# Kernel optimization log

Hardware: AMD Instinct MI355X
Metric: run time of the kernel (lower is better)

## Reference

```python
import jax, jax.numpy as jnp
import numpy as np

N_HEAD = 16
THETA = 10000.0


def _freqs_cos_sin(head_dim, seq_len):
    # matches precompute_freqs_cis: freqs = 1/theta^(arange(0,dim,2)/dim), outer with t
    inv = 1.0 / (THETA ** (jnp.arange(0, head_dim, 2, dtype=jnp.float32) / head_dim))
    t = jnp.arange(seq_len, dtype=jnp.float32)
    ang = jnp.outer(t, inv)  # [L, head_dim//2]
    return jnp.cos(ang), jnp.sin(ang)


def _rope(x, cos, sin):
    # x: [B, H, L, D]; pairs are interleaved (view_as_complex on (..., D//2, 2))
    x1 = x[..., 0::2]
    x2 = x[..., 1::2]
    out_re = x1 * cos - x2 * sin
    out_im = x1 * sin + x2 * cos
    return jnp.stack([out_re, out_im], axis=-1).reshape(x.shape)


def setup_inputs() -> dict:
    key = jax.random.key(0)
    ks = jax.random.split(key, 11)
    B, L, D = 2, 2048, 1024
    s = 0.02
    return {
        "q": jax.random.normal(ks[0], (B, L, D), jnp.float32),
        "k": jax.random.normal(ks[1], (B, L, D), jnp.float32),
        "v": jax.random.normal(ks[2], (B, L, D), jnp.float32),
        "wq": jax.random.normal(ks[3], (D, D), jnp.float32) * s,
        "bq": jax.random.normal(ks[4], (D,), jnp.float32) * s,
        "wk": jax.random.normal(ks[5], (D, D), jnp.float32) * s,
        "bk": jax.random.normal(ks[6], (D,), jnp.float32) * s,
        "wv": jax.random.normal(ks[7], (D, D), jnp.float32) * s,
        "bv": jax.random.normal(ks[8], (D,), jnp.float32) * s,
        "wo": jax.random.normal(ks[9], (D, D), jnp.float32) * s,
        "bo": jax.random.normal(ks[10], (D,), jnp.float32) * s,
    }


def reference(q, k, v, wq, bq, wk, bk, wv, bv, wo, bo):
    B, L, D = q.shape
    Hd = D // N_HEAD
    # projections (nn.Linear: x @ W^T + b)
    qp = q @ wq.T + bq
    kp = k @ wk.T + bk
    vp = v @ wv.T + bv
    # split: [B, L, D] -> [B, H, L, Hd]
    def split(t):
        return t.reshape(B, L, N_HEAD, Hd).transpose(0, 2, 1, 3)
    qh, kh, vh = split(qp), split(kp), split(vp)
    cos, sin = _freqs_cos_sin(Hd, L)  # [L, Hd//2], broadcasts over B, H
    qh = _rope(qh, cos, sin)
    kh = _rope(kh, cos, sin)
    # scaled dot-product attention (no mask)
    scores = jnp.einsum("bhqd,bhkd->bhqk", qh, kh) / jnp.sqrt(jnp.float32(Hd))
    attn = jax.nn.softmax(scores, axis=-1)
    out = jnp.einsum("bhqk,bhkd->bhqd", attn, vh)
    # concat heads and output projection
    out = out.transpose(0, 2, 1, 3).reshape(B, L, D)
    return out @ wo.T + bo
```

## Files before the change

### kernel.cpp

```cpp
#include <hip/hip_runtime.h>
#include <hip/hip_bf16.h>
#include <math.h>

#define BB 2
#define LL 2048
#define DD 1024
#define NH 16
#define HD 64

typedef short v8s __attribute__((ext_vector_type(8)));
typedef float v4f __attribute__((ext_vector_type(4)));
typedef float v16f __attribute__((ext_vector_type(16)));

__device__ __forceinline__ float b2f(unsigned short b) {
  union { unsigned int u; float f; } c; c.u = ((unsigned int)b) << 16; return c.f;
}
__device__ __forceinline__ unsigned short f2b(float x) {
  union { float f; unsigned int u; } c; c.f = x;
  unsigned int u = c.u;
  u += 0x7fffu + ((u >> 16) & 1u);
  return (unsigned short)(u >> 16);
}
__device__ __forceinline__ unsigned int asu(float x) {
  union { float f; unsigned int u; } c; c.f = x; return c.u;
}
__device__ __forceinline__ unsigned int pk2(float lo, float hi) {
  return __builtin_amdgcn_perm(asu(hi), asu(lo), 0x07060302u);
}

#if defined(__has_builtin)
#if __has_builtin(__builtin_amdgcn_exp2f)
#define EXP2(x) __builtin_amdgcn_exp2f(x)
#else
#define EXP2(x) __expf((x) * 0.69314718056f)
#endif
#else
#define EXP2(x) __expf((x) * 0.69314718056f)
#endif

__device__ __forceinline__ void gload16(const void* g, void* l) {
  __builtin_amdgcn_global_load_lds(
      (const __attribute__((address_space(1))) void*)g,
      (__attribute__((address_space(3))) void*)l, 16, 0, 0);
}

#define VM_WAIT4 do { asm volatile("s_waitcnt vmcnt(4)" ::: "memory"); \
                      __builtin_amdgcn_sched_barrier(0); } while (0)
#define VM_WAIT0 do { asm volatile("s_waitcnt vmcnt(0)" ::: "memory"); \
                      __builtin_amdgcn_sched_barrier(0); } while (0)
#define SBAR     do { __builtin_amdgcn_s_barrier(); \
                      __builtin_amdgcn_sched_barrier(0); } while (0)

struct CastArgs { const float* s[7]; unsigned short* d[7]; float* ct; float* st; };
__global__ void cast_all(CastArgs a) {
  int z = blockIdx.z;
  if (z == 16) {
    if (blockIdx.x >= 256) return;
    int id = blockIdx.x * blockDim.x + threadIdx.x;
    int t = id >> 5, i = id & 31;
    float inv = powf(10000.0f, -(float)(2 * i) / 64.0f);
    float ang = (float)t * inv;
    a.ct[id] = cosf(ang);
    a.st[id] = sinf(ang);
    return;
  }
  int t = (z < 12) ? (z >> 2) : (z - 9);
  int off = (z < 12) ? ((z & 3) << 18) : 0;
  int i = off + blockIdx.x * blockDim.x + threadIdx.x;
  float4 v = ((const float4*)a.s[t])[i];
  ushort4 o;
  o.x = f2b(v.x); o.y = f2b(v.y); o.z = f2b(v.z); o.w = f2b(v.w);
  ((ushort4*)a.d[t])[i] = o;
}

__device__ __forceinline__ size_t ring_src_off(int id, int row0, int Kd) {
  int sr = id >> 3, slot = id & 7;
  int g = slot ^ (sr & 7);
  int r = (sr << 1) | (g >> 2), c = g & 3;
  return (size_t)(row0 + r) * Kd + c * 8;
}
__device__ __forceinline__ int ring_frag_off(int row, int quad) {
  int sr = row >> 1;
  int slot = (((row & 1) << 2) | quad) ^ (sr & 7);
  return sr * 64 + slot * 8;
}

__device__ __forceinline__ void ring_gemm_core(
    const unsigned short* __restrict__ X, const unsigned short* __restrict__ W,
    unsigned short* LDS_, int bm0, int bn0, v4f acc[4][4]) {
  const int K = DD;
  const int tid = threadIdx.x;
  const int lane = tid & 63, wave = tid >> 6;
  const int quad = lane >> 4, l16 = lane & 15;
  const int wm = (wave >> 1) * 64, wn = (wave & 1) * 64;

  const unsigned short* aS0 = X + ring_src_off(tid, bm0, K);
  const unsigned short* aS1 = X + ring_src_off(256 + tid, bm0, K);
  const unsigned short* bS0 = W + ring_src_off(tid, bn0, K);
  const unsigned short* bS1 = W + ring_src_off(256 + tid, bn0, K);

  int aoff[4], boff[4];
#pragma unroll
  for (int i = 0; i < 4; ++i) {
    aoff[i] = ring_frag_off(wm + i * 16 + l16, quad);
    boff[i] = ring_frag_off(wn + i * 16 + l16, quad);
  }

  auto stage = [&](int q, int kofs) {
    unsigned short* Ab = &LDS_[q * 4096];
    unsigned short* Bb = &LDS_[12288 + q * 4096];
    gload16(aS0 + kofs, &Ab[tid * 8]);
    gload16(aS1 + kofs, &Ab[(256 + tid) * 8]);
    gload16(bS0 + kofs, &Bb[tid * 8]);
    gload16(bS1 + kofs, &Bb[(256 + tid) * 8]);
  };
  auto compute = [&](int q) {
    const unsigned short* Ab = &LDS_[q * 4096];
    const unsigned short* Bb = &LDS_[12288 + q * 4096];
    v8s a[4], b[4];
#pragma unroll
    for (int i = 0; i < 4; ++i) {
      a[i] = *(const v8s*)&Ab[aoff[i]];
      b[i] = *(const v8s*)&Bb[boff[i]];
    }
#pragma unroll
    for (int mi = 0; mi < 4; ++mi)
#pragma unroll
      for (int ni = 0; ni < 4; ++ni)
        acc[mi][ni] = __builtin_amdgcn_mfma_f32_16x16x32_bf16(a[mi], b[ni], acc[mi][ni], 0, 0, 0);
  };

  const int nt = K / 32;
  stage(0, 0);
  stage(1, 32);
  VM_WAIT4;
  SBAR;
  int cur = 0, s2 = 2, kofs = 64;
#pragma unroll 1
  for (int t = 0; t < nt - 2; ++t) {
    stage(s2, kofs);
    compute(cur);
    VM_WAIT4;
    SBAR;
    cur = (cur == 2) ? 0 : cur + 1;
    s2 = (s2 == 2) ? 0 : s2 + 1;
    kofs += 32;
  }
  compute(cur);
  VM_WAIT0;
  SBAR;
  cur = (cur == 2) ? 0 : cur + 1;
  compute(cur);
}

__global__ __launch_bounds__(256, 3) void gemm_qkv(
    const unsigned short* __restrict__ qb, const unsigned short* __restrict__ kb,
    const unsigned short* __restrict__ vb,
    const unsigned short* __restrict__ wqb, const unsigned short* __restrict__ wkb,
    const unsigned short* __restrict__ wvb,
    const float* __restrict__ bq, const float* __restrict__ bk,
    const float* __restrict__ bv_,
    unsigned short* __restrict__ qp, unsigned short* __restrict__ khh,
    unsigned short* __restrict__ vt,
    const float* __restrict__ ctab, const float* __restrict__ stab) {
  __shared__ __align__(16) unsigned short LDS_[24576];
  const int z = blockIdx.z;
  const unsigned short* X = (z == 0) ? qb : (z == 1) ? kb : vb;
  const unsigned short* W = (z == 0) ? wqb : (z == 1) ? wkb : wvb;
  const float* bias = (z == 0) ? bq : (z == 1) ? bk : bv_;
  const int N = DD;
  const int tid = threadIdx.x;
  const int lane = tid & 63, wave = tid >> 6;
  const int quad = lane >> 4, l16 = lane & 15;
  const int bm0 = blockIdx.x * 128;
  const int bn0 = blockIdx.y * 128;
  const int wm = (wave >> 1) * 64, wn = (wave & 1) * 64;

  const v4f vzero = {0.f, 0.f, 0.f, 0.f};
  v4f acc[4][4];
#pragma unroll
  for (int i = 0; i < 4; ++i)
#pragma unroll
    for (int j = 0; j < 4; ++j) acc[i][j] = vzero;

  ring_gemm_core(X, W, LDS_, bm0, bn0, acc);

  float bv[4];
#pragma unroll
  for (int ni = 0; ni < 4; ++ni) bv[ni] = bias[bn0 + wn + ni * 16 + l16];

  if (z < 2) {
    const float scl = (z == 0) ? 0.18033688f : 1.0f;
    const int h = (bn0 + wn) >> 6;
    const float sgn = (l16 & 1) ? 1.0f : -1.0f;
#pragma unroll
    for (int mi = 0; mi < 4; ++mi) {
#pragma unroll
      for (int r = 0; r < 4; ++r) {
        int row = bm0 + wm + mi * 16 + quad * 4 + r;
        int l = row & (LL - 1);
        int bidx = row >> 11;
        size_t baseq = (size_t)row * N + bn0 + wn + l16;
        size_t basek = ((size_t)(bidx * NH + h) * LL + l) * HD + l16;
#pragma unroll
        for (int ni = 0; ni < 4; ++ni) {
          int ii = (ni * 16 + l16) >> 1;
          float c = ctab[l * 32 + ii], s = stab[l * 32 + ii];
          float v = acc[mi][ni][r] + bv[ni];
          float vp = __shfl_xor(v, 1);
          float o = (v * c + sgn * (vp * s)) * scl;
          if (z == 0) qp[baseq + ni * 16] = f2b(o);
          else        khh[basek + ni * 16] = f2b(o);
        }
      }
    }
  } else {
    __syncthreads();
    unsigned short* T = LDS_;
#pragma unroll
    for (int mi = 0; mi < 4; ++mi)
#pragma unroll
      for (int r = 0; r < 4; ++r) {
        int tl = wm + mi * 16 + quad * 4 + r;
        int tlp = (tl & ~12) | ((tl & 4) << 1) | ((tl & 8) >> 1);
        int chunk = tlp >> 3, offw = tlp & 7;
#pragma unroll
        for (int ni = 0; ni < 4; ++ni) {
          int fl = wn + ni * 16 + l16;
          T[fl * 128 + ((chunk ^ (fl & 15)) * 8) + offw] =
              f2b(acc[mi][ni][r] + bv[ni]);
        }
      }
    __syncthreads();
    int fl = tid >> 1, half = tid & 1;
    int fg = bn0 + fl;
    int h2 = fg >> 6, d = fg & 63;
    int bidx = bm0 >> 11, l0 = bm0 & (LL - 1);
    unsigned short* dst =
        vt + (((size_t)(bidx * NH + h2) * HD + d) * LL) + l0 + half * 64;
#pragma unroll
    for (int i = 0; i < 8; ++i) {
      int chunk = half * 8 + i;
      int slot = chunk ^ (fl & 15);
      *(v8s*)(dst + i * 8) = *(const v8s*)&T[fl * 128 + slot * 8];
    }
  }
}

__global__ __launch_bounds__(256, 3) void gemm_out(
    const unsigned short* __restrict__ x, const unsigned short* __restrict__ w,
    const float* __restrict__ b, float* __restrict__ y) {
  __shared__ __align__(16) unsigned short LDS_[24576];
  const int N = DD;
  const int tid = threadIdx.x;
  const int lane = tid & 63, wave = tid >> 6;
  const int quad = lane >> 4, l16 = lane & 15;
  const int bm0 = blockIdx.x * 128;
  const int bn0 = blockIdx.y * 128;
  const int wm = (wave >> 1) * 64, wn = (wave & 1) * 64;

  const v4f vzero = {0.f, 0.f, 0.f, 0.f};
  v4f acc[4][4];
#pragma unroll
  for (int i = 0; i < 4; ++i)
#pragma unroll
    for (int j = 0; j < 4; ++j) acc[i][j] = vzero;

  ring_gemm_core(x, w, LDS_, bm0, bn0, acc);

  float bv[4];
#pragma unroll
  for (int ni = 0; ni < 4; ++ni) bv[ni] = b[bn0 + wn + ni * 16 + l16];
#pragma unroll
  for (int mi = 0; mi < 4; ++mi) {
#pragma unroll
    for (int r = 0; r < 4; ++r) {
      int row = bm0 + wm + mi * 16 + quad * 4 + r;
      size_t base = (size_t)row * N + bn0 + wn + l16;
#pragma unroll
      for (int ni = 0; ni < 4; ++ni)
        y[base + ni * 16] = acc[mi][ni][r] + bv[ni];
    }
  }
}

__global__ __launch_bounds__(256, 3) void flash_kernel(
    const unsigned short* __restrict__ qp,
    const unsigned short* __restrict__ kh,
    const unsigned short* __restrict__ vt,
    unsigned short* __restrict__ attn) {
  __shared__ __align__(16) unsigned short S_[24576];
  const int tid = threadIdx.x, wave = tid >> 6, lane = tid & 63;
  const int l32 = lane & 31, hf = lane >> 5;
  const int bh = blockIdx.x, b = bh >> 4, hd = bh & 15;
  const int q0 = blockIdx.y * 128;
  const unsigned short* kbase = kh + (size_t)bh * LL * HD;
  const unsigned short* vbase = vt + (size_t)bh * HD * LL;

  const int qrow = q0 + wave * 32 + l32;
  v8s qf[4];
  {
    const unsigned short* qsrc = qp + ((size_t)(b * LL + qrow) * DD + hd * HD);
#pragma unroll
    for (int ks2 = 0; ks2 < 4; ++ks2)
      qf[ks2] = *(const v8s*)(qsrc + ks2 * 16 + hf * 8);
  }

  const int r0 = tid >> 3, s0 = tid & 7;
  const int r1 = (256 + tid) >> 3;
  const unsigned short* kS0 = kbase + (size_t)r0 * HD + (s0 ^ (r0 & 7)) * 8;
  const unsigned short* kS1 = kbase + (size_t)r1 * HD + (s0 ^ (r1 & 7)) * 8;
  const unsigned short* vS0 = vbase + (size_t)r0 * LL + (s0 ^ (r0 & 7)) * 8;
  const unsigned short* vS1 = vbase + (size_t)r1 * LL + (s0 ^ (r1 & 7)) * 8;

  v16f o0, o1;
#pragma unroll
  for (int i = 0; i < 16; ++i) { o0[i] = 0.0f; o1[i] = 0.0f; }
  float ls = 0.0f;

  auto stage = [&](int q, int t) {
    unsigned short* Kb = &S_[q * 8192];
    unsigned short* Vb = &S_[q * 8192 + 4096];
    gload16(kS0 + (size_t)t * 4096, &Kb[tid * 8]);
    gload16(kS1 + (size_t)t * 4096, &Kb[(256 + tid) * 8]);
    gload16(vS0 + t * 64, &Vb[tid * 8]);
    gload16(vS1 + t * 64, &Vb[(256 + tid) * 8]);
  };

  auto compute = [&](int q) {
    const unsigned short* Ks = &S_[q * 8192];
    const unsigned short* Vs = &S_[q * 8192 + 4096];
#pragma unroll
    for (int g = 0; g < 2; ++g) {
      v16f sc;
#pragma unroll
      for (int i = 0; i < 16; ++i) sc[i] = 0.0f;
#pragma unroll
      for (int ks2 = 0; ks2 < 4; ++ks2) {
        int row = g * 32 + l32;
        int slot = (ks2 * 2 + hf) ^ (row & 7);
        v8s kf = *(const v8s*)&Ks[row * 64 + slot * 8];
        sc = __builtin_amdgcn_mfma_f32_32x32x16_bf16(kf, qf[ks2], sc, 0, 0, 0);
      }
      v16f e;
#pragma unroll
      for (int i = 0; i < 16; ++i) e[i] = EXP2(sc[i]);
      float t0 = (e[0] + e[1]) + (e[2] + e[3]);
      float t1 = (e[4] + e[5]) + (e[6] + e[7]);
      float t2 = (e[8] + e[9]) + (e[10] + e[11]);
      float t3 = (e[12] + e[13]) + (e[14] + e[15]);
      ls += (t0 + t1) + (t2 + t3);
#pragma unroll
      for (int k2 = 0; k2 < 2; ++k2) {
        union { v8s v; unsigned int u[4]; } pb;
#pragma unroll
        for (int a = 0; a < 4; ++a)
          pb.u[a] = pk2(e[8 * k2 + 2 * a], e[8 * k2 + 2 * a + 1]);
        int k16 = g * 2 + k2;
        int slotv = (k16 * 2 + hf) ^ (l32 & 7);
        v8s vf0 = *(const v8s*)&Vs[l32 * 64 + slotv * 8];
        v8s vf1 = *(const v8s*)&Vs[(32 + l32) * 64 + slotv * 8];
        o0 = __builtin_amdgcn_mfma_f32_32x32x16_bf16(vf0, pb.v, o0, 0, 0, 0);
        o1 = __builtin_amdgcn_mfma_f32_32x32x16_bf16(vf1, pb.v, o1, 0, 0, 0);
      }
    }
  };

  const int nt = LL / 64;
  stage(0, 0);
  stage(1, 1);
  VM_WAIT4;
  SBAR;
  int cur = 0, s2 = 2;
#pragma unroll 1
  for (int t = 0; t < nt - 2; ++t) {
    stage(s2, t + 2);
    compute(cur);
    VM_WAIT4;
    SBAR;
    cur = (cur == 2) ? 0 : cur + 1;
    s2 = (s2 == 2) ? 0 : s2 + 1;
  }
  compute(cur);
  VM_WAIT0;
  SBAR;
  cur = (cur == 2) ? 0 : cur + 1;
  compute(cur);

  ls += __shfl_xor(ls, 32);
  float inv = 1.0f / ls;

  unsigned short* Wt = S_ + wave * 2048;
#pragma unroll
  for (int dt = 0; dt < 2; ++dt)
#pragma unroll
    for (int r = 0; r < 16; ++r) {
      int dl = (r & 3) + 8 * (r >> 2) + 4 * hf;
      int d = dt * 32 + dl;
      int chunk = d >> 3, offw = d & 7;
      int slot = chunk ^ (l32 & 7);
      float val = (dt == 0) ? o0[r] : o1[r];
      Wt[l32 * 64 + slot * 8 + offw] = f2b(val * inv);
    }
#pragma unroll
  for (int i = 0; i < 4; ++i) {
    int qr = lane >> 1;
    int chunk = (lane & 1) * 4 + i;
    int slot = chunk ^ (qr & 7);
    v8s dv = *(const v8s*)&Wt[qr * 64 + slot * 8];
    int token = q0 + wave * 32 + qr;
    *(v8s*)(attn + ((size_t)(b * LL + token) * DD) + hd * HD + chunk * 8) = dv;
  }
}

extern "C" void kernel_launch(void* const* d_in, const int* in_sizes, int n_in,
                              void* d_out, int out_size, void* d_ws, size_t ws_size,
                              hipStream_t stream) {
  const float* q  = (const float*)d_in[0];
  const float* k  = (const float*)d_in[1];
  const float* v  = (const float*)d_in[2];
  const float* wq = (const float*)d_in[3];
  const float* bq = (const float*)d_in[4];
  const float* wk = (const float*)d_in[5];
  const float* bk = (const float*)d_in[6];
  const float* wv = (const float*)d_in[7];
  const float* bv = (const float*)d_in[8];
  const float* wo = (const float*)d_in[9];
  const float* bo = (const float*)d_in[10];
  float* out = (float*)d_out;

  size_t off = 0;
  char* wsb = (char*)d_ws;
  auto take = [&](size_t n) { void* p = wsb + off; off += n; return p; };
  const size_t SZT = (size_t)BB * LL * DD * 2;
  const size_t SZW = (size_t)DD * DD * 2;
  unsigned short* qb   = (unsigned short*)take(SZT);
  unsigned short* kb   = (unsigned short*)take(SZT);
  unsigned short* vb   = (unsigned short*)take(SZT);
  unsigned short* wqb  = (unsigned short*)take(SZW);
  unsigned short* wkb  = (unsigned short*)take(SZW);
  unsigned short* wvb  = (unsigned short*)take(SZW);
  unsigned short* wob  = (unsigned short*)take(SZW);
  unsigned short* qp   = (unsigned short*)take(SZT);
  unsigned short* khh  = (unsigned short*)take(SZT);
  unsigned short* vtt  = (unsigned short*)take(SZT);
  unsigned short* attn = (unsigned short*)take(SZT);
  float* ctab = (float*)take((size_t)LL * 32 * 4);
  float* stab = (float*)take((size_t)LL * 32 * 4);

  CastArgs ca;
  ca.s[0] = q;  ca.s[1] = k;  ca.s[2] = v;  ca.s[3] = wq;
  ca.s[4] = wk; ca.s[5] = wv; ca.s[6] = wo;
  ca.d[0] = qb;  ca.d[1] = kb;  ca.d[2] = vb;  ca.d[3] = wqb;
  ca.d[4] = wkb; ca.d[5] = wvb; ca.d[6] = wob;
  ca.ct = ctab; ca.st = stab;
  cast_all<<<dim3(1024, 1, 17), 256, 0, stream>>>(ca);

  gemm_qkv<<<dim3(BB * LL / 128, DD / 128, 3), 256, 0, stream>>>(
      qb, kb, vb, wqb, wkb, wvb, bq, bk, bv, qp, khh, vtt, ctab, stab);

  flash_kernel<<<dim3(BB * NH, LL / 128), 256, 0, stream>>>(
      qp, khh, vtt, attn);

  gemm_out<<<dim3(BB * LL / 128, DD / 128, 1), 256, 0, stream>>>(attn, wob, bo, out);
}
```

Before: 211.8 us.

## Restructure flash inner loop: preload K/V fragments, interleave MFMAs, set wave priority

The per-tile compute now loads all K and V fragments from LDS up front, then issues the two 32-row QK^T MFMA chains interleaved and runs both exponentials together before the PV MFMAs. s_setprio raises wave priority around the MFMA bursts so that matrix work from different waves overlaps with other waves' exp and LDS phases. The extra live registers lead to lowering launch bounds from 3 to 2 waves-per-EU, which trades occupancy for more independent instructions per wave.

Measured after the change: 210.3 us. No clear change (-0.7%).

```diff
diff --git a/kernel.cpp b/kernel.cpp
--- a/kernel.cpp
+++ b/kernel.cpp
@@ -284,7 +284,7 @@
   }
 }
 
-__global__ __launch_bounds__(256, 3) void flash_kernel(
+__global__ __launch_bounds__(256, 2) void flash_kernel(
     const unsigned short* __restrict__ qp,
     const unsigned short* __restrict__ kh,
     const unsigned short* __restrict__ vt,
@@ -330,40 +330,62 @@
   auto compute = [&](int q) {
     const unsigned short* Ks = &S_[q * 8192];
     const unsigned short* Vs = &S_[q * 8192 + 4096];
-#pragma unroll
-    for (int g = 0; g < 2; ++g) {
-      v16f sc;
-#pragma unroll
-      for (int i = 0; i < 16; ++i) sc[i] = 0.0f;
-#pragma unroll
-      for (int ks2 = 0; ks2 < 4; ++ks2) {
-        int row = g * 32 + l32;
-        int slot = (ks2 * 2 + hf) ^ (row & 7);
-        v8s kf = *(const v8s*)&Ks[row * 64 + slot * 8];
-        sc = __builtin_amdgcn_mfma_f32_32x32x16_bf16(kf, qf[ks2], sc, 0, 0, 0);
-      }
-      v16f e;
-#pragma unroll
-      for (int i = 0; i < 16; ++i) e[i] = EXP2(sc[i]);
-      float t0 = (e[0] + e[1]) + (e[2] + e[3]);
-      float t1 = (e[4] + e[5]) + (e[6] + e[7]);
-      float t2 = (e[8] + e[9]) + (e[10] + e[11]);
-      float t3 = (e[12] + e[13]) + (e[14] + e[15]);
-      ls += (t0 + t1) + (t2 + t3);
-#pragma unroll
-      for (int k2 = 0; k2 < 2; ++k2) {
-        union { v8s v; unsigned int u[4]; } pb;
-#pragma unroll
-        for (int a = 0; a < 4; ++a)
-          pb.u[a] = pk2(e[8 * k2 + 2 * a], e[8 * k2 + 2 * a + 1]);
-        int k16 = g * 2 + k2;
-        int slotv = (k16 * 2 + hf) ^ (l32 & 7);
-        v8s vf0 = *(const v8s*)&Vs[l32 * 64 + slotv * 8];
-        v8s vf1 = *(const v8s*)&Vs[(32 + l32) * 64 + slotv * 8];
-        o0 = __builtin_amdgcn_mfma_f32_32x32x16_bf16(vf0, pb.v, o0, 0, 0, 0);
-        o1 = __builtin_amdgcn_mfma_f32_32x32x16_bf16(vf1, pb.v, o1, 0, 0, 0);
-      }
-    }
+    const int row0 = l32, row1 = 32 + l32;
+    v8s kf0[4], kf1[4];
+#pragma unroll
+    for (int ks2 = 0; ks2 < 4; ++ks2) {
+      kf0[ks2] = *(const v8s*)&Ks[row0 * 64 + (((ks2 * 2 + hf) ^ (row0 & 7)) * 8)];
+      kf1[ks2] = *(const v8s*)&Ks[row1 * 64 + (((ks2 * 2 + hf) ^ (row1 & 7)) * 8)];
+    }
+    v8s vfa[4], vfb[4];
+#pragma unroll
+    for (int k16 = 0; k16 < 4; ++k16) {
+      int slotv = (k16 * 2 + hf) ^ (l32 & 7);
+      vfa[k16] = *(const v8s*)&Vs[l32 * 64 + slotv * 8];
+      vfb[k16] = *(const v8s*)&Vs[(32 + l32) * 64 + slotv * 8];
+    }
+    v16f sc0, sc1;
+#pragma unroll
+    for (int i = 0; i < 16; ++i) { sc0[i] = 0.0f; sc1[i] = 0.0f; }
+    __builtin_amdgcn_s_setprio(1);
+#pragma unroll
+    for (int ks2 = 0; ks2 < 4; ++ks2) {
+      sc0 = __builtin_amdgcn_mfma_f32_32x32x16_bf16(kf0[ks2], qf[ks2], sc0, 0, 0, 0);
+      sc1 = __builtin_amdgcn_mfma_f32_32x32x16_bf16(kf1[ks2], qf[ks2], sc1, 0, 0, 0);
+    }
+    __builtin_amdgcn_s_setprio(0);
+    v16f e0, e1;
+#pragma unroll
+    for (int i = 0; i < 16; ++i) e0[i] = EXP2(sc0[i]);
+#pragma unroll
+    for (int i = 0; i < 16; ++i) e1[i] = EXP2(sc1[i]);
+    float s00 = (e0[0] + e0[1]) + (e0[2] + e0[3]);
+    float s01 = (e0[4] + e0[5]) + (e0[6] + e0[7]);
+    float s02 = (e0[8] + e0[9]) + (e0[10] + e0[11]);
+    float s03 = (e0[12] + e0[13]) + (e0[14] + e0[15]);
+    float s10 = (e1[0] + e1[1]) + (e1[2] + e1[3]);
+    float s11 = (e1[4] + e1[5]) + (e1[6] + e1[7]);
+    float s12 = (e1[8] + e1[9]) + (e1[10] + e1[11]);
+    float s13 = (e1[12] + e1[13]) + (e1[14] + e1[15]);
+    ls += ((s00 + s01) + (s02 + s03)) + ((s10 + s11) + (s12 + s13));
+    union { v8s v; unsigned int u[4]; } pb0, pb1, pb2, pb3;
+#pragma unroll
+    for (int a = 0; a < 4; ++a) {
+      pb0.u[a] = pk2(e0[2 * a], e0[2 * a + 1]);
+      pb1.u[a] = pk2(e0[8 + 2 * a], e0[8 + 2 * a + 1]);
+      pb2.u[a] = pk2(e1[2 * a], e1[2 * a + 1]);
+      pb3.u[a] = pk2(e1[8 + 2 * a], e1[8 + 2 * a + 1]);
+    }
+    __builtin_amdgcn_s_setprio(1);
+    o0 = __builtin_amdgcn_mfma_f32_32x32x16_bf16(vfa[0], pb0.v, o0, 0, 0, 0);
+    o1 = __builtin_amdgcn_mfma_f32_32x32x16_bf16(vfb[0], pb0.v, o1, 0, 0, 0);
+    o0 = __builtin_amdgcn_mfma_f32_32x32x16_bf16(vfa[1], pb1.v, o0, 0, 0, 0);
+    o1 = __builtin_amdgcn_mfma_f32_32x32x16_bf16(vfb[1], pb1.v, o1, 0, 0, 0);
+    o0 = __builtin_amdgcn_mfma_f32_32x32x16_bf16(vfa[2], pb2.v, o0, 0, 0, 0);
+    o1 = __builtin_amdgcn_mfma_f32_32x32x16_bf16(vfb[2], pb2.v, o1, 0, 0, 0);
+    o0 = __builtin_amdgcn_mfma_f32_32x32x16_bf16(vfa[3], pb3.v, o0, 0, 0, 0);
+    o1 = __builtin_amdgcn_mfma_f32_32x32x16_bf16(vfb[3], pb3.v, o1, 0, 0, 0);
+    __builtin_amdgcn_s_setprio(0);
   };
 
   const int nt = LL / 64;
```

## Split flash attention over key halves with a separate combine kernel

Applied to the files above, without the earlier changes.

The flash attention kernel is split along the key dimension into two halves (a grid z dimension of 2). Each block handles 1024 keys with 32-key tiles and a smaller LDS footprint, which allows higher occupancy. Each half writes its unnormalised bf16 partial output and row sums into reused workspace, and a new combine kernel adds the halves, normalises and writes the head layout. This doubles the block count to fill more CUs, at the cost of an extra launch, partial-output traffic and extra bf16 rounding of the partials.

New measurement: 220.4 us. 4.0% more time.

```diff
diff --git a/kernel.cpp b/kernel.cpp
--- a/kernel.cpp
+++ b/kernel.cpp
@@ -45,6 +45,8 @@
 }
 
 #define VM_WAIT4 do { asm volatile("s_waitcnt vmcnt(4)" ::: "memory"); \
+                      __builtin_amdgcn_sched_barrier(0); } while (0)
+#define VM_WAIT2 do { asm volatile("s_waitcnt vmcnt(2)" ::: "memory"); \
                       __builtin_amdgcn_sched_barrier(0); } while (0)
 #define VM_WAIT0 do { asm volatile("s_waitcnt vmcnt(0)" ::: "memory"); \
                       __builtin_amdgcn_sched_barrier(0); } while (0)
@@ -284,18 +286,20 @@
   }
 }
 
-__global__ __launch_bounds__(256, 3) void flash_kernel(
+__global__ __launch_bounds__(256, 4) void flash_split(
     const unsigned short* __restrict__ qp,
     const unsigned short* __restrict__ kh,
     const unsigned short* __restrict__ vt,
-    unsigned short* __restrict__ attn) {
-  __shared__ __align__(16) unsigned short S_[24576];
+    unsigned short* __restrict__ opart,
+    float* __restrict__ lspart) {
+  __shared__ __align__(16) unsigned short S_[12288];
   const int tid = threadIdx.x, wave = tid >> 6, lane = tid & 63;
   const int l32 = lane & 31, hf = lane >> 5;
   const int bh = blockIdx.x, b = bh >> 4, hd = bh & 15;
-  const int q0 = blockIdx.y * 128;
-  const unsigned short* kbase = kh + (size_t)bh * LL * HD;
-  const unsigned short* vbase = vt + (size_t)bh * HD * LL;
+  const int qt = blockIdx.y, ks = blockIdx.z;
+  const int q0 = qt * 128;
+  const unsigned short* kbase = kh + (size_t)bh * LL * HD + (size_t)ks * 1024 * HD;
+  const unsigned short* vbase = vt + (size_t)bh * HD * LL + ks * 1024;
 
   const int qrow = q0 + wave * 32 + l32;
   v8s qf[4];
@@ -306,12 +310,10 @@
       qf[ks2] = *(const v8s*)(qsrc + ks2 * 16 + hf * 8);
   }
 
-  const int r0 = tid >> 3, s0 = tid & 7;
-  const int r1 = (256 + tid) >> 3;
-  const unsigned short* kS0 = kbase + (size_t)r0 * HD + (s0 ^ (r0 & 7)) * 8;
-  const unsigned short* kS1 = kbase + (size_t)r1 * HD + (s0 ^ (r1 & 7)) * 8;
-  const unsigned short* vS0 = vbase + (size_t)r0 * LL + (s0 ^ (r0 & 7)) * 8;
-  const unsigned short* vS1 = vbase + (size_t)r1 * LL + (s0 ^ (r1 & 7)) * 8;
+  const int rk = tid >> 3, sk = tid & 7;
+  const int rv = tid >> 2, sv = tid & 3;
+  const unsigned short* kS = kbase + (size_t)rk * HD + ((sk ^ (rk & 7)) * 8);
+  const unsigned short* vS = vbase + (size_t)rv * LL + ((sv ^ (rv & 3)) * 8);
 
   v16f o0, o1;
 #pragma unroll
@@ -319,64 +321,58 @@
   float ls = 0.0f;
 
   auto stage = [&](int q, int t) {
-    unsigned short* Kb = &S_[q * 8192];
-    unsigned short* Vb = &S_[q * 8192 + 4096];
-    gload16(kS0 + (size_t)t * 4096, &Kb[tid * 8]);
-    gload16(kS1 + (size_t)t * 4096, &Kb[(256 + tid) * 8]);
-    gload16(vS0 + t * 64, &Vb[tid * 8]);
-    gload16(vS1 + t * 64, &Vb[(256 + tid) * 8]);
+    gload16(kS + t * 2048, &S_[q * 4096 + tid * 8]);
+    gload16(vS + t * 32, &S_[q * 4096 + 2048 + tid * 8]);
   };
 
   auto compute = [&](int q) {
-    const unsigned short* Ks = &S_[q * 8192];
-    const unsigned short* Vs = &S_[q * 8192 + 4096];
-#pragma unroll
-    for (int g = 0; g < 2; ++g) {
-      v16f sc;
-#pragma unroll
-      for (int i = 0; i < 16; ++i) sc[i] = 0.0f;
-#pragma unroll
-      for (int ks2 = 0; ks2 < 4; ++ks2) {
-        int row = g * 32 + l32;
-        int slot = (ks2 * 2 + hf) ^ (row & 7);
-        v8s kf = *(const v8s*)&Ks[row * 64 + slot * 8];
-        sc = __builtin_amdgcn_mfma_f32_32x32x16_bf16(kf, qf[ks2], sc, 0, 0, 0);
-      }
-      v16f e;
-#pragma unroll
-      for (int i = 0; i < 16; ++i) e[i] = EXP2(sc[i]);
-      float t0 = (e[0] + e[1]) + (e[2] + e[3]);
-      float t1 = (e[4] + e[5]) + (e[6] + e[7]);
-      float t2 = (e[8] + e[9]) + (e[10] + e[11]);
-      float t3 = (e[12] + e[13]) + (e[14] + e[15]);
-      ls += (t0 + t1) + (t2 + t3);
-#pragma unroll
-      for (int k2 = 0; k2 < 2; ++k2) {
-        union { v8s v; unsigned int u[4]; } pb;
-#pragma unroll
-        for (int a = 0; a < 4; ++a)
-          pb.u[a] = pk2(e[8 * k2 + 2 * a], e[8 * k2 + 2 * a + 1]);
-        int k16 = g * 2 + k2;
-        int slotv = (k16 * 2 + hf) ^ (l32 & 7);
-        v8s vf0 = *(const v8s*)&Vs[l32 * 64 + slotv * 8];
-        v8s vf1 = *(const v8s*)&Vs[(32 + l32) * 64 + slotv * 8];
-        o0 = __builtin_amdgcn_mfma_f32_32x32x16_bf16(vf0, pb.v, o0, 0, 0, 0);
-        o1 = __builtin_amdgcn_mfma_f32_32x32x16_bf16(vf1, pb.v, o1, 0, 0, 0);
-      }
-    }
+    const unsigned short* Ks = &S_[q * 4096];
+    const unsigned short* Vs = Ks + 2048;
+    v16f sc;
+#pragma unroll
+    for (int i = 0; i < 16; ++i) sc[i] = 0.0f;
+#pragma unroll
+    for (int ks2 = 0; ks2 < 4; ++ks2) {
+      v8s kf = *(const v8s*)&Ks[l32 * 64 + (((ks2 * 2 + hf) ^ (l32 & 7)) * 8)];
+      sc = __builtin_amdgcn_mfma_f32_32x32x16_bf16(kf, qf[ks2], sc, 0, 0, 0);
+    }
+    v16f e;
+#pragma unroll
+    for (int i = 0; i < 16; ++i) e[i] = EXP2(sc[i]);
+    float t0 = (e[0] + e[1]) + (e[2] + e[3]);
+    float t1 = (e[4] + e[5]) + (e[6] + e[7]);
+    float t2 = (e[8] + e[9]) + (e[10] + e[11]);
+    float t3 = (e[12] + e[13]) + (e[14] + e[15]);
+    ls += (t0 + t1) + (t2 + t3);
+    union { v8s v; unsigned int u[4]; } pb0, pb1;
+#pragma unroll
+    for (int a = 0; a < 4; ++a) {
+      pb0.u[a] = pk2(e[2 * a], e[2 * a + 1]);
+      pb1.u[a] = pk2(e[8 + 2 * a], e[8 + 2 * a + 1]);
+    }
+    int slot0 = (hf) ^ (l32 & 3);
+    int slot1 = (2 + hf) ^ (l32 & 3);
+    v8s vfa0 = *(const v8s*)&Vs[l32 * 32 + slot0 * 8];
+    v8s vfb0 = *(const v8s*)&Vs[(32 + l32) * 32 + slot0 * 8];
+    v8s vfa1 = *(const v8s*)&Vs[l32 * 32 + slot1 * 8];
+    v8s vfb1 = *(const v8s*)&Vs[(32 + l32) * 32 + slot1 * 8];
+    o0 = __builtin_amdgcn_mfma_f32_32x32x16_bf16(vfa0, pb0.v, o0, 0, 0, 0);
+    o1 = __builtin_amdgcn_mfma_f32_32x32x16_bf16(vfb0, pb0.v, o1, 0, 0, 0);
+    o0 = __builtin_amdgcn_mfma_f32_32x32x16_bf16(vfa1, pb1.v, o0, 0, 0, 0);
+    o1 = __builtin_amdgcn_mfma_f32_32x32x16_bf16(vfb1, pb1.v, o1, 0, 0, 0);
   };
 
-  const int nt = LL / 64;
+  const int nt = 32;
   stage(0, 0);
   stage(1, 1);
-  VM_WAIT4;
+  VM_WAIT2;
   SBAR;
   int cur = 0, s2 = 2;
 #pragma unroll 1
   for (int t = 0; t < nt - 2; ++t) {
     stage(s2, t + 2);
     compute(cur);
-    VM_WAIT4;
+    VM_WAIT2;
     SBAR;
     cur = (cur == 2) ? 0 : cur + 1;
     s2 = (s2 == 2) ? 0 : s2 + 1;
@@ -387,20 +383,45 @@
   cur = (cur == 2) ? 0 : cur + 1;
   compute(cur);
 
-  ls += __shfl_xor(ls, 32);
-  float inv = 1.0f / ls;
-
-  unsigned short* Wt = S_ + wave * 2048;
+  const int blk4 = ((bh * 16 + qt) * 2 + ks) * 4 + wave;
+  lspart[blk4 * 64 + lane] = ls;
+  unsigned short* ob = opart + (size_t)blk4 * 2048;
+#pragma unroll
+  for (int r = 0; r < 16; ++r) {
+    ob[r * 64 + lane] = f2b(o0[r]);
+    ob[(16 + r) * 64 + lane] = f2b(o1[r]);
+  }
+}
+
+__global__ __launch_bounds__(256) void flash_combine(
+    const unsigned short* __restrict__ opart, const float* __restrict__ lspart,
+    unsigned short* __restrict__ attn) {
+  __shared__ __align__(16) unsigned short W_[8192];
+  const int tid = threadIdx.x, wave = tid >> 6, lane = tid & 63;
+  const int l32 = lane & 31, hf = lane >> 5;
+  const int bh = blockIdx.x, b = bh >> 4, hd = bh & 15;
+  const int qt = blockIdx.y, q0 = qt * 128;
+
+  const int p0 = ((bh * 16 + qt) * 2 + 0) * 4 + wave;
+  const int p1 = p0 + 4;
+  float lsv = lspart[p0 * 64 + lane] + lspart[p1 * 64 + lane];
+  lsv += __shfl_xor(lsv, 32);
+  float inv = 1.0f / lsv;
+
+  const unsigned short* oa = opart + (size_t)p0 * 2048;
+  const unsigned short* ob = opart + (size_t)p1 * 2048;
+  unsigned short* Wt = W_ + wave * 2048;
 #pragma unroll
   for (int dt = 0; dt < 2; ++dt)
 #pragma unroll
     for (int r = 0; r < 16; ++r) {
+      int idx = (dt * 16 + r) * 64 + lane;
+      float val = (b2f(oa[idx]) + b2f(ob[idx])) * inv;
       int dl = (r & 3) + 8 * (r >> 2) + 4 * hf;
       int d = dt * 32 + dl;
       int chunk = d >> 3, offw = d & 7;
       int slot = chunk ^ (l32 & 7);
-      float val = (dt == 0) ? o0[r] : o1[r];
-      Wt[l32 * 64 + slot * 8 + offw] = f2b(val * inv);
+      Wt[l32 * 64 + slot * 8 + offw] = f2b(val);
     }
 #pragma unroll
   for (int i = 0; i < 4; ++i) {
@@ -448,6 +469,9 @@
   float* ctab = (float*)take((size_t)LL * 32 * 4);
   float* stab = (float*)take((size_t)LL * 32 * 4);
 
+  unsigned short* opart = qb;
+  float* lspart = (float*)wqb;
+
   CastArgs ca;
   ca.s[0] = q;  ca.s[1] = k;  ca.s[2] = v;  ca.s[3] = wq;
   ca.s[4] = wk; ca.s[5] = wv; ca.s[6] = wo;
@@ -459,8 +483,11 @@
   gemm_qkv<<<dim3(BB * LL / 128, DD / 128, 3), 256, 0, stream>>>(
       qb, kb, vb, wqb, wkb, wvb, bq, bk, bv, qp, khh, vtt, ctab, stab);
 
-  flash_kernel<<<dim3(BB * NH, LL / 128), 256, 0, stream>>>(
-      qp, khh, vtt, attn);
+  flash_split<<<dim3(BB * NH, LL / 128, 2), 256, 0, stream>>>(
+      qp, khh, vtt, opart, lspart);
+
+  flash_combine<<<dim3(BB * NH, LL / 128), 256, 0, stream>>>(
+      opart, lspart, attn);
 
   gemm_out<<<dim3(BB * LL / 128, DD / 128, 1), 256, 0, stream>>>(attn, wob, bo, out);
 }
```
